# Performance work log

Measured on AMD Instinct MI355X. Metric: run time of the kernel, lower is better.

Reference implementation:

```python
import jax, jax.numpy as jnp
import numpy as np

V = 32000   # input_size (vocab)
H = 768     # hidden_size
C = 256     # condition_size
HC = H + C  # h_c_size
L = 2048    # sequence length


def _lstm_step(x, h, c, W_ih, W_hh, b_ih, b_hh):
    # PyTorch LSTM gate order: i, f, g, o
    gates = x @ W_ih.T + b_ih + h @ W_hh.T + b_hh  # [4*HC]
    i, f, g, o = jnp.split(gates, 4)
    c_new = jax.nn.sigmoid(f) * c + jax.nn.sigmoid(i) * jnp.tanh(g)
    h_new = jax.nn.sigmoid(o) * jnp.tanh(c_new)
    return h_new, c_new


def setup_inputs() -> dict:
    key = jax.random.key(0)
    ks = iter(jax.random.split(key, 40))
    p = lambda shape: (jax.random.normal(next(ks), shape, dtype=jnp.float32) * 0.02)
    inp = {
        "input": jax.random.randint(next(ks), (1, L), 0, V, dtype=jnp.int64),
        "condition": jax.random.randint(next(ks), (1,), 0, 4, dtype=jnp.int64),
        "eps_h": jax.random.normal(next(ks), (H,), dtype=jnp.float32),
        "eps_c": jax.random.normal(next(ks), (H,), dtype=jnp.float32),
        "kld_weight": jax.random.uniform(next(ks), (1,), dtype=jnp.float32),
        # encoder params
        "enc_embed": p((V, HC)),
        "enc_cond_embed": p((4, C)),
        "enc_W_ih": p((4 * HC, HC)), "enc_W_hh": p((4 * HC, HC)),
        "enc_b_ih": p((4 * HC,)), "enc_b_hh": p((4 * HC,)),
        "fc_mh_w": p((H, HC)), "fc_mh_b": p((H,)),
        "fc_lh_w": p((H, HC)), "fc_lh_b": p((H,)),
        "fc_mc_w": p((H, HC)), "fc_mc_b": p((H,)),
        "fc_lc_w": p((H, HC)), "fc_lc_b": p((H,)),
        # decoder params
        "dec_embed": p((V, HC)),
        "dec_cond_embed": p((4, C)),
        "dec_W_ih": p((4 * HC, HC)), "dec_W_hh": p((4 * HC, HC)),
        "dec_b_ih": p((4 * HC,)), "dec_b_hh": p((4 * HC,)),
        "fc_h_w": p((H, HC)), "fc_h_b": p((H,)),
        "fc_c_w": p((H, HC)), "fc_c_b": p((H,)),
        "out_w": p((V, HC)), "out_b": p((V,)),
    }
    return inp


def reference(input, condition, eps_h, eps_c, kld_weight,
              enc_embed, enc_cond_embed, enc_W_ih, enc_W_hh, enc_b_ih, enc_b_hh,
              fc_mh_w, fc_mh_b, fc_lh_w, fc_lh_b, fc_mc_w, fc_mc_b, fc_lc_w, fc_lc_b,
              dec_embed, dec_cond_embed, dec_W_ih, dec_W_hh, dec_b_ih, dec_b_hh,
              fc_h_w, fc_h_b, fc_c_w, fc_c_b, out_w, out_b):
    tokens = input[0]          # [L]
    cond = condition[0]

    # ---- Encoder over tokens[1:-1] ----
    x_seq = enc_embed[tokens[1:-1]]              # [L-2, HC]
    c_emb = enc_cond_embed[cond]                 # [C]
    h0 = jnp.concatenate([jnp.zeros((H,), jnp.float32), c_emb])  # [HC]
    c0 = h0

    def enc_step(carry, x):
        h, c = carry
        h, c = _lstm_step(x, h, c, enc_W_ih, enc_W_hh, enc_b_ih, enc_b_hh)
        return (h, c), None

    (hT, cT), _ = jax.lax.scan(enc_step, (h0, c0), x_seq)

    m_h = hT @ fc_mh_w.T + fc_mh_b
    lv_h = hT @ fc_lh_w.T + fc_lh_b
    z_h = eps_h * jnp.exp(lv_h * 0.5) + m_h      # [H]
    m_c = cT @ fc_mc_w.T + fc_mc_b
    lv_c = cT @ fc_lc_w.T + fc_lc_b
    z_c = eps_c * jnp.exp(lv_c * 0.5) + m_c

    kl_h = 0.5 * jnp.sum(m_h ** 2 + jnp.exp(lv_h) - 1.0 - lv_h)
    kl_c = 0.5 * jnp.sum(m_c ** 2 + jnp.exp(lv_c) - 1.0 - lv_c)

    # ---- Decoder, teacher forcing over L-1 steps ----
    dec_x = dec_embed[tokens[:-1]]               # [L-1, HC]
    targets = tokens[1:]                         # [L-1]
    cd = dec_cond_embed[cond]                    # [C]

    def dec_step(carry, xt):
        h, c = carry                             # [H], [H]
        x, tgt = xt
        hc = jnp.concatenate([h, cd])            # [HC]
        cc = jnp.concatenate([c, cd])
        h_new, c_new = _lstm_step(x, hc, cc, dec_W_ih, dec_W_hh, dec_b_ih, dec_b_hh)
        logits = h_new @ out_w.T + out_b         # [V]
        ce = -jax.nn.log_softmax(logits)[tgt]
        h2 = h_new @ fc_h_w.T + fc_h_b
        c2 = c_new @ fc_c_w.T + fc_c_b
        return (h2, c2), ce

    _, ces = jax.lax.scan(dec_step, (z_h, z_c), (dec_x, targets))
    reconst = jnp.mean(ces)
    loss = reconst + (kl_h + kl_c) * kld_weight[0]
    return jnp.stack([loss, reconst, kl_h, kl_c])
```

## Files before the change

kernel.cpp:

```cpp
#include <hip/hip_runtime.h>
#include <math.h>

#define VSZ 32000
#define Hh  768
#define Cc  256
#define HCd 1024
#define G4  4096
#define NSE 2046
#define NSD 2047

#define EB 64
#define ET 512

typedef __attribute__((ext_vector_type(4))) unsigned uint4v;
typedef __attribute__((ext_vector_type(2))) unsigned uint2v;
typedef __attribute__((ext_vector_type(8))) short bf16x8;
typedef __attribute__((ext_vector_type(4))) float f32x4;

__device__ __forceinline__ float sigmoidf_(float x){ return 1.0f/(1.0f+expf(-x)); }

__device__ __forceinline__ float wave_reduce(float v){
#pragma unroll
  for(int o=32;o;o>>=1) v += __shfl_xor(v,o,64);
  return v;
}

__device__ __forceinline__ float redl0(float v){
  int x;
  x=__builtin_amdgcn_update_dpp(0,__float_as_int(v),0xB1,0xf,0xf,true); v+=__int_as_float(x);
  x=__builtin_amdgcn_update_dpp(0,__float_as_int(v),0x4E,0xf,0xf,true); v+=__int_as_float(x);
  v+=__int_as_float(__builtin_amdgcn_ds_swizzle(__float_as_int(v),0x101F));
  v+=__int_as_float(__builtin_amdgcn_ds_swizzle(__float_as_int(v),0x201F));
  v+=__int_as_float(__builtin_amdgcn_ds_swizzle(__float_as_int(v),0x401F));
  v+=__int_as_float(__builtin_amdgcn_readlane(__float_as_int(v),32));
  return v;
}

__device__ __forceinline__ uint4v ld_uc4(const unsigned* p){
  uint4v r;
  asm volatile("global_load_dwordx4 %0, %1, off sc0 sc1\n\ts_waitcnt vmcnt(0)"
               : "=v"(r) : "v"(p) : "memory");
  return r;
}
__device__ __forceinline__ uint2v ld_uc2(const unsigned* p){
  uint2v r;
  asm volatile("global_load_dwordx2 %0, %1, off sc0 sc1\n\ts_waitcnt vmcnt(0)"
               : "=v"(r) : "v"(p) : "memory");
  return r;
}
__device__ __forceinline__ void st_uc4(unsigned* p, uint4v v){
  asm volatile("global_store_dwordx4 %0, %1, off sc0 sc1" :: "v"(p), "v"(v) : "memory");
}
__device__ __forceinline__ void st_uc2(unsigned* p, uint2v v){
  asm volatile("global_store_dwordx2 %0, %1, off sc0 sc1" :: "v"(p), "v"(v) : "memory");
}

__device__ __forceinline__ unsigned pk_bf16(float a, float b){
  unsigned ua=__float_as_uint(a); ua += 0x7fffu + ((ua>>16)&1u);
  unsigned ub=__float_as_uint(b); ub += 0x7fffu + ((ub>>16)&1u);
  return (ua>>16) | (ub & 0xffff0000u);
}

__global__ void k_init3(unsigned* estate, const float* __restrict__ cemb,
                        const int* __restrict__ condp){
  int tid=threadIdx.x;
  int cond=condp[0];
  for(int i=tid;i<HCd;i+=256){
    float v=(i<Hh)?0.f:cemb[cond*Cc+(i-Hh)];
    estate[i]=__float_as_uint(v)&~1u;
    estate[HCd+i]=1u;
  }
}

__global__ __launch_bounds__(256) void k_dconst(const float* __restrict__ Whh,
    const float* __restrict__ fhb, const float* __restrict__ cemb,
    const int* __restrict__ condp, float* __restrict__ cvec){
  int lane=threadIdx.x&63, wv=threadIdx.x>>6;
  int wgid=blockIdx.x*4+wv;
  int cond=condp[0];
  for(int r=wgid;r<G4;r+=256){
    const float* row=Whh+(size_t)r*HCd;
    float s=0.f;
    for(int k=lane;k<Hh;k+=64) s+=row[k]*fhb[k];
    for(int k=lane;k<Cc;k+=64) s+=row[Hh+k]*cemb[cond*Cc+k];
    s=wave_reduce(s);
    if(lane==0) cvec[r]=s;
  }
}

#define GBM 128
#define GBN 128
#define GBK 16

__global__ __launch_bounds__(256) void k_weff(const float* __restrict__ A,
    const float* __restrict__ B, float* __restrict__ Cm){
  __shared__ float As[GBK][GBM];
  __shared__ float Bs[GBK][GBN];
  int tid=threadIdx.x;
  int m0=blockIdx.x*GBM, n0=blockIdx.y*GBN;
  int tm=tid>>4, tn=tid&15;
  float acc[8][8]={};
  for(int k0=0;k0<Hh;k0+=GBK){
#pragma unroll
    for(int u=0;u<2;u++){
      int idx=tid*2+u;
      int row=idx>>2, q=idx&3;
      float4 v=*(const float4*)(A+(size_t)(m0+row)*HCd + k0+q*4);
      As[q*4+0][row]=v.x; As[q*4+1][row]=v.y; As[q*4+2][row]=v.z; As[q*4+3][row]=v.w;
      int kk=idx>>5, nc=idx&31;
      float4 w=*(const float4*)(B+(size_t)(k0+kk)*HCd + n0+nc*4);
      *(float4*)&Bs[kk][nc*4]=w;
    }
    __syncthreads();
#pragma unroll
    for(int kk=0;kk<GBK;kk++){
      float a[8],b[8];
      *(float4*)&a[0]=*(float4*)&As[kk][tm*8]; *(float4*)&a[4]=*(float4*)&As[kk][tm*8+4];
      *(float4*)&b[0]=*(float4*)&Bs[kk][tn*8]; *(float4*)&b[4]=*(float4*)&Bs[kk][tn*8+4];
#pragma unroll
      for(int i=0;i<8;i++)
#pragma unroll
        for(int j=0;j<8;j++) acc[i][j]+=a[i]*b[j];
    }
    __syncthreads();
  }
#pragma unroll
  for(int i=0;i<8;i++)
#pragma unroll
    for(int j=0;j<8;j++)
      Cm[(size_t)(m0+tm*8+i)*HCd + n0+tn*8+j]=acc[i][j];
}

__global__ __launch_bounds__(256) void k_xgemm(
    const float* __restrict__ emb, const float* __restrict__ Wih,
    const float* __restrict__ b1, const float* __restrict__ b2,
    const int* __restrict__ tok, int tshift, int M,
    float* __restrict__ X)
{
  __shared__ float As[GBK][GBM];
  __shared__ float Bs[GBK][GBN];
  int tid=threadIdx.x;
  int m0=blockIdx.x*GBM, n0=blockIdx.y*GBN;
  int tm=tid>>4, tn=tid&15;
  int arow=m0+(tid>>1);
  int atok=(arow<M)?tok[arow+tshift]:0;
  const float* abase=emb+(size_t)atok*HCd+(tid&1)*8;
  const float* bbase=Wih+(size_t)(n0+(tid>>1))*HCd+(tid&1)*8;
  int srow=tid>>1;
  float acc[8][8]={};
  for(int k0=0;k0<HCd;k0+=GBK){
#pragma unroll
    for(int u=0;u<2;u++){
      int q=2*(tid&1)+u;
      float4 v={0,0,0,0};
      if(arow<M) v=*(const float4*)(abase+k0+u*4);
      As[q*4+0][srow]=v.x; As[q*4+1][srow]=v.y; As[q*4+2][srow]=v.z; As[q*4+3][srow]=v.w;
      float4 w=*(const float4*)(bbase+k0+u*4);
      Bs[q*4+0][srow]=w.x; Bs[q*4+1][srow]=w.y; Bs[q*4+2][srow]=w.z; Bs[q*4+3][srow]=w.w;
    }
    __syncthreads();
#pragma unroll
    for(int kk=0;kk<GBK;kk++){
      float a[8],b[8];
      *(float4*)&a[0]=*(float4*)&As[kk][tm*8]; *(float4*)&a[4]=*(float4*)&As[kk][tm*8+4];
      *(float4*)&b[0]=*(float4*)&Bs[kk][tn*8]; *(float4*)&b[4]=*(float4*)&Bs[kk][tn*8+4];
#pragma unroll
      for(int i=0;i<8;i++)
#pragma unroll
        for(int j=0;j<8;j++) acc[i][j]+=a[i]*b[j];
    }
    __syncthreads();
  }
#pragma unroll
  for(int i=0;i<8;i++){
    int m=m0+tm*8+i; if(m>=M) continue;
#pragma unroll
    for(int j=0;j<8;j++){
      int n=n0+tn*8+j;
      X[(size_t)m*G4+n]=acc[i][j]+b1[n]+b2[n];
    }
  }
}

#define TBM 128
#define TBN 128
#define TBK 32

__global__ __launch_bounds__(256) void k_xgemm_mfma(
    const float* __restrict__ emb, const float* __restrict__ Wih,
    const float* __restrict__ b1, const float* __restrict__ b2,
    const int* __restrict__ tok, int M, float* __restrict__ X)
{
  __shared__ ushort As[TBM*TBK];
  __shared__ ushort Bs[TBN*TBK];
  int tid=threadIdx.x;
  int m0=blockIdx.x*TBM, n0=blockIdx.y*TBN;
  int wid=tid>>6, lane=tid&63;
  int wm=wid>>1, wn=wid&1;
  int r15=lane&15, g=lane>>4;
  f32x4 acc[4][4]={};
  int srow=tid>>1, shalf=tid&1;
  int arow=m0+srow;
  int atok=(arow<M)?tok[arow]:0;
  const float* aptr=emb+(size_t)atok*HCd + shalf*16;
  const float* bptr=Wih+(size_t)(n0+srow)*HCd + shalf*16;
  bool aok=arow<M;
  float bj[4];
#pragma unroll
  for(int j=0;j<4;j++){ int n=n0+wn*64+j*16+r15; bj[j]=b1[n]+b2[n]; }

  for(int k0=0;k0<HCd;k0+=TBK){
    float4 va0={0,0,0,0},va1={0,0,0,0},va2={0,0,0,0},va3={0,0,0,0};
    if(aok){
      va0=*(const float4*)(aptr+k0);   va1=*(const float4*)(aptr+k0+4);
      va2=*(const float4*)(aptr+k0+8); va3=*(const float4*)(aptr+k0+12);
    }
    float4 vb0=*(const float4*)(bptr+k0),   vb1=*(const float4*)(bptr+k0+4);
    float4 vb2=*(const float4*)(bptr+k0+8), vb3=*(const float4*)(bptr+k0+12);
    uint4v pa0={pk_bf16(va0.x,va0.y),pk_bf16(va0.z,va0.w),pk_bf16(va1.x,va1.y),pk_bf16(va1.z,va1.w)};
    uint4v pa1={pk_bf16(va2.x,va2.y),pk_bf16(va2.z,va2.w),pk_bf16(va3.x,va3.y),pk_bf16(va3.z,va3.w)};
    uint4v pb0={pk_bf16(vb0.x,vb0.y),pk_bf16(vb0.z,vb0.w),pk_bf16(vb1.x,vb1.y),pk_bf16(vb1.z,vb1.w)};
    uint4v pb1={pk_bf16(vb2.x,vb2.y),pk_bf16(vb2.z,vb2.w),pk_bf16(vb3.x,vb3.y),pk_bf16(vb3.z,vb3.w)};
    int sx=(srow>>1)&3;
    int u0=(shalf*2+0)^sx, u1=(shalf*2+1)^sx;
    *(uint4v*)&As[srow*32+u0*8]=pa0; *(uint4v*)&As[srow*32+u1*8]=pa1;
    *(uint4v*)&Bs[srow*32+u0*8]=pb0; *(uint4v*)&Bs[srow*32+u1*8]=pb1;
    __syncthreads();
    bf16x8 af[4], bf[4];
#pragma unroll
    for(int i=0;i<4;i++){
      int ra=wm*64+i*16+r15;
      af[i]=*(const bf16x8*)&As[ra*32+((g^((ra>>1)&3))<<3)];
      int rb=wn*64+i*16+r15;
      bf[i]=*(const bf16x8*)&Bs[rb*32+((g^((rb>>1)&3))<<3)];
    }
#pragma unroll
    for(int i=0;i<4;i++)
#pragma unroll
      for(int j=0;j<4;j++)
        acc[i][j]=__builtin_amdgcn_mfma_f32_16x16x32_bf16(af[i],bf[j],acc[i][j],0,0,0);
    __syncthreads();
  }
#pragma unroll
  for(int i=0;i<4;i++){
    int grow0=m0+wm*64+i*16+g*4;
#pragma unroll
    for(int j=0;j<4;j++){
      int gcol=n0+wn*64+j*16+r15;
#pragma unroll
      for(int r=0;r<4;r++){
        int grow=grow0+r;
        if(grow<M) X[(size_t)grow*G4+gcol]=acc[i][j][r]+bj[j];
      }
    }
  }
}

__global__ __launch_bounds__(ET,2) void k_enc3(
    const float* __restrict__ Xg,
    const float* __restrict__ Whh,
    unsigned* estate,
    float* hT, float* cT)
{
  __shared__ float hlds[2][HCd];
  const int tid=threadIdx.x, lane=tid&63, wv=tid>>6;
  const int wid=blockIdx.x*8+wv;
  const int j0=wid*2, j1=j0+1;
  float w[8][16];
#pragma unroll
  for(int q=0;q<4;q++)
#pragma unroll
    for(int jj=0;jj<2;jj++){
      const float* p=Whh+(size_t)(q*HCd+j0+jj)*HCd+lane;
#pragma unroll
      for(int e=0;e<16;e++) w[q*2+jj][e]=p[(size_t)e*64];
    }
  float xg[8];
#pragma unroll
  for(int r=0;r<8;r++) xg[r]=Xg[(r>>1)*HCd+j0+(r&1)];
  float c0=0.f,c1=0.f;
  const int i0=tid*2, i1=i0+1;

  for(int s=1;s<=NSE;s++){
    uint2v v;
    unsigned* src=estate+((s-1)&1)*HCd;
    if(s==1){ v.x=src[i0]; v.y=src[i1]; }
    else{
      const unsigned expp=(unsigned)(((s-1)>>1)&1);
      for(;;){
        v=ld_uc2(src+i0);
        if((((v.x^expp)|(v.y^expp))&1u)==0u) break;
        __builtin_amdgcn_s_sleep(1);
      }
    }
    float* hl=hlds[(s-1)&1];
    hl[i0]=__uint_as_float(v.x); hl[i1]=__uint_as_float(v.y);
    __syncthreads();
    if(s==1){ c0=hl[j0]; c1=hl[j1]; }
    float hseg[16];
#pragma unroll
    for(int e=0;e<16;e++) hseg[e]=hl[lane+64*e];
    float d[8];
#pragma unroll
    for(int r=0;r<8;r++){ float sacc=0.f;
#pragma unroll
      for(int e=0;e<16;e++) sacc+=w[r][e]*hseg[e];
      d[r]=sacc; }
#pragma unroll
    for(int r=0;r<8;r++) d[r]=redl0(d[r]);
    float gi0=d[0]+xg[0], gi1=d[1]+xg[1];
    float gf0=d[2]+xg[2], gf1=d[3]+xg[3];
    float gg0=d[4]+xg[4], gg1=d[5]+xg[5];
    float go0=d[6]+xg[6], go1=d[7]+xg[7];
    if(s<NSE){
      const float* px=Xg+(size_t)s*G4;
#pragma unroll
      for(int r=0;r<8;r++) xg[r]=px[(r>>1)*HCd+j0+(r&1)];
    }
    c0=sigmoidf_(gf0)*c0+sigmoidf_(gi0)*tanhf(gg0);
    float h0=sigmoidf_(go0)*tanhf(c0);
    c1=sigmoidf_(gf1)*c1+sigmoidf_(gi1)*tanhf(gg1);
    float h1=sigmoidf_(go1)*tanhf(c1);
    unsigned wpar=(unsigned)((s>>1)&1);
    if(lane==0){
      uint2v pk;
      pk.x=(__float_as_uint(h0)&~1u)|wpar;
      pk.y=(__float_as_uint(h1)&~1u)|wpar;
      st_uc2(estate+(s&1)*HCd+j0,pk);
      if(s==NSE){ hT[j0]=h0; hT[j1]=h1; cT[j0]=c0; cT[j1]=c1; }
    }
  }
}

__global__ __launch_bounds__(256) void k_head(
    const float* __restrict__ hT, const float* __restrict__ cT,
    const float* __restrict__ mhw, const float* __restrict__ mhb,
    const float* __restrict__ lhw, const float* __restrict__ lhb,
    const float* __restrict__ mcw, const float* __restrict__ mcb,
    const float* __restrict__ lcw, const float* __restrict__ lcb,
    const float* __restrict__ eps_h, const float* __restrict__ eps_c,
    const float* __restrict__ cemb, const int* __restrict__ condp,
    unsigned* dstate0, float* klh, float* klc)
{
  int i=blockIdx.x;
  int tid=threadIdx.x, lane=tid&63, wv=tid>>6;
  __shared__ float sm[4];
  const float* Wm=(wv==0)?mhw:(wv==1)?lhw:(wv==2)?mcw:lcw;
  const float* vec=(wv<2)?hT:cT;
  const float* row=Wm+(size_t)i*HCd;
  float s=0.f;
  for(int k=lane;k<HCd;k+=64) s+=row[k]*vec[k];
  s=wave_reduce(s);
  if(lane==0) sm[wv]=s;
  __syncthreads();
  if(tid==0){
    float mh=sm[0]+mhb[i], lh=sm[1]+lhb[i];
    float mc=sm[2]+mcb[i], lc=sm[3]+lcb[i];
    float zhv=eps_h[i]*expf(lh*0.5f)+mh;
    float zcv=eps_c[i]*expf(lc*0.5f)+mc;
    dstate0[2*i]  =__float_as_uint(zhv)&~1u;
    dstate0[2*i+1]=__float_as_uint(zcv)&~1u;
    klh[i]=0.5f*(mh*mh+expf(lh)-1.f-lh);
    klc[i]=0.5f*(mc*mc+expf(lc)-1.f-lc);
    if(i<Cc){
      unsigned cu=__float_as_uint(cemb[condp[0]*Cc+i])&~1u;
      dstate0[2*(Hh+i)]=cu; dstate0[2*(Hh+i)+1]=cu;
    }
  }
}

__global__ __launch_bounds__(256) void k_dec0(
    const float* __restrict__ Xg, const float* __restrict__ WhhO,
    const unsigned* __restrict__ dstate0, unsigned* dstate1, float* Hmat)
{
  int tid=threadIdx.x, lane=tid&63, wv=tid>>6;
  int j=blockIdx.x*4+wv;
  float hseg[16];
#pragma unroll
  for(int e=0;e<16;e++) hseg[e]=__uint_as_float(dstate0[2*(lane+64*e)]);
  float g[4];
#pragma unroll
  for(int q=0;q<4;q++){
    const float* p=WhhO+(size_t)(q*HCd+j)*HCd+lane;
    float s=0.f;
#pragma unroll
    for(int e=0;e<16;e++) s+=p[(size_t)e*64]*hseg[e];
    s=wave_reduce(s);
    g[q]=s+Xg[q*HCd+j];
  }
  float cc=__uint_as_float(dstate0[2*j+1]);
  float cn=sigmoidf_(g[1])*cc+sigmoidf_(g[0])*tanhf(g[2]);
  float hn=sigmoidf_(g[3])*tanhf(cn);
  if(lane==0){
    dstate1[2*j]  =__float_as_uint(hn)&~1u;
    dstate1[2*j+1]=__float_as_uint(cn)&~1u;
    Hmat[j]=hn;
  }
}

__global__ __launch_bounds__(ET,2) void k_dec3(
    const float* __restrict__ Xg,
    const float* __restrict__ Weff,
    const float* __restrict__ cvec,
    const float* __restrict__ fccw, const float* __restrict__ fccb,
    const float* __restrict__ cemb, const int* __restrict__ condp,
    unsigned* dstate, float* __restrict__ Hmat)
{
  __shared__ float hlds[2][HCd];
  __shared__ float clds[2][HCd];
  const int tid=threadIdx.x, lane=tid&63, wv=tid>>6;
  const int wid=blockIdx.x*8+wv;
  const int j0=wid*2, j1=j0+1;
  float w[8][16];
#pragma unroll
  for(int q=0;q<4;q++)
#pragma unroll
    for(int jj=0;jj<2;jj++){
      const float* p=Weff+(size_t)(q*HCd+j0+jj)*HCd+lane;
#pragma unroll
      for(int e=0;e<16;e++) w[q*2+jj][e]=p[(size_t)e*64];
    }
  const bool hasf=(j0<Hh);
  float fcc0[16], fcc1[16];
  if(hasf){
    const float* p0=fccw+(size_t)j0*HCd+lane;
    const float* p1=fccw+(size_t)j1*HCd+lane;
#pragma unroll
    for(int e=0;e<16;e++){ fcc0[e]=p0[(size_t)e*64]; fcc1[e]=p1[(size_t)e*64]; }
  } else {
#pragma unroll
    for(int e=0;e<16;e++){ fcc0[e]=0.f; fcc1[e]=0.f; }
  }
  float fb0=hasf?fccb[j0]:0.f, fb1=hasf?fccb[j1]:0.f;
  int cond=condp[0];
  float cd0=hasf?0.f:cemb[cond*Cc+(j0-Hh)];
  float cd1=hasf?0.f:cemb[cond*Cc+(j1-Hh)];
  float cv[8];
#pragma unroll
  for(int r=0;r<8;r++) cv[r]=cvec[(r>>1)*HCd+j0+(r&1)];
  float xg[8];
  { const float* px=Xg+(size_t)1*G4;
#pragma unroll
    for(int r=0;r<8;r++) xg[r]=px[(r>>1)*HCd+j0+(r&1)]; }
  const int i0=tid*2, i1=i0+1;

  for(int s=2;s<=NSD;s++){
    uint4v v;
    unsigned* st=dstate+((s-1)&1)*2*HCd;
    if(s==2){ v=*(const uint4v*)(st+4*tid); }
    else{
      const unsigned expp=(unsigned)(((s-1)>>1)&1);
      for(;;){
        v=ld_uc4(st+4*tid);
        if((((v.x^expp)|(v.y^expp)|(v.z^expp)|(v.w^expp))&1u)==0u) break;
        __builtin_amdgcn_s_sleep(1);
      }
    }
    float* hl=hlds[(s-1)&1]; float* cl=clds[(s-1)&1];
    hl[i0]=__uint_as_float(v.x); cl[i0]=__uint_as_float(v.y);
    hl[i1]=__uint_as_float(v.z); cl[i1]=__uint_as_float(v.w);
    __syncthreads();
    float hseg[16], cseg[16];
#pragma unroll
    for(int e=0;e<16;e++){ hseg[e]=hl[lane+64*e]; cseg[e]=cl[lane+64*e]; }
    float d[8]; float s8=0.f, s9=0.f;
#pragma unroll
    for(int r=0;r<8;r++){ float sacc=0.f;
#pragma unroll
      for(int e=0;e<16;e++) sacc+=w[r][e]*hseg[e];
      d[r]=sacc; }
#pragma unroll
    for(int r=0;r<8;r++) d[r]=redl0(d[r]);
    if(hasf){
#pragma unroll
      for(int e=0;e<16;e++){ s8+=fcc0[e]*cseg[e]; s9+=fcc1[e]*cseg[e]; }
      s8=redl0(s8); s9=redl0(s9);
    }
    float gi0=d[0]+xg[0]+cv[0], gi1=d[1]+xg[1]+cv[1];
    float gf0=d[2]+xg[2]+cv[2], gf1=d[3]+xg[3]+cv[3];
    float gg0=d[4]+xg[4]+cv[4], gg1=d[5]+xg[5]+cv[5];
    float go0=d[6]+xg[6]+cv[6], go1=d[7]+xg[7]+cv[7];
    if(s<NSD){
      const float* px=Xg+(size_t)s*G4;
#pragma unroll
      for(int r=0;r<8;r++) xg[r]=px[(r>>1)*HCd+j0+(r&1)];
    }
    float cc0=hasf?(s8+fb0):cd0;
    float cc1=hasf?(s9+fb1):cd1;
    float cn0=sigmoidf_(gf0)*cc0+sigmoidf_(gi0)*tanhf(gg0);
    float hn0=sigmoidf_(go0)*tanhf(cn0);
    float cn1=sigmoidf_(gf1)*cc1+sigmoidf_(gi1)*tanhf(gg1);
    float hn1=sigmoidf_(go1)*tanhf(cn1);
    unsigned wpar=(unsigned)((s>>1)&1);
    if(lane==0){
      uint4v pk;
      pk.x=(__float_as_uint(hn0)&~1u)|wpar;
      pk.y=(__float_as_uint(cn0)&~1u)|wpar;
      pk.z=(__float_as_uint(hn1)&~1u)|wpar;
      pk.w=(__float_as_uint(cn1)&~1u)|wpar;
      st_uc4(dstate+(s&1)*2*HCd+2*j0,pk);
      Hmat[(size_t)(s-1)*HCd+j0]=hn0; Hmat[(size_t)(s-1)*HCd+j1]=hn1;
    }
  }
}

__global__ __launch_bounds__(256) void k_cvtB(const float* __restrict__ B,
    unsigned* __restrict__ Bb){
  size_t idx=(size_t)blockIdx.x*256+threadIdx.x;
  size_t total=(size_t)VSZ*HCd/4;
  for(size_t i=idx;i<total;i+=(size_t)gridDim.x*256){
    float4 v=*(const float4*)(B+i*4);
    Bb[i*2]  =pk_bf16(v.x,v.y);
    Bb[i*2+1]=pk_bf16(v.z,v.w);
  }
}

__global__ __launch_bounds__(256) void k_gemm2(
    const float* __restrict__ A, const ushort* __restrict__ Bb,
    const float* __restrict__ bias, float* __restrict__ Cm, int M)
{
  __shared__ ushort As[TBM*TBK];
  __shared__ ushort Bs[TBN*TBK];
  int tid=threadIdx.x;
  int m0=blockIdx.x*TBM, n0=blockIdx.y*TBN;
  int wid=tid>>6, lane=tid&63;
  int wm=wid>>1, wn=wid&1;
  int r15=lane&15, g=lane>>4;
  f32x4 acc[4][4]={};
  int srow=tid>>1, shalf=tid&1;
  const float*  aptr=A +(size_t)(m0+srow)*HCd + shalf*16;
  const ushort* bptr=Bb+(size_t)(n0+srow)*HCd + shalf*16;
  bool aok=(m0+srow)<M;
  float bj[4];
#pragma unroll
  for(int j=0;j<4;j++) bj[j]=bias[n0+wn*64+j*16+r15];

  for(int k0=0;k0<HCd;k0+=TBK){
    float4 va0={0,0,0,0},va1={0,0,0,0},va2={0,0,0,0},va3={0,0,0,0};
    if(aok){
      va0=*(const float4*)(aptr+k0);   va1=*(const float4*)(aptr+k0+4);
      va2=*(const float4*)(aptr+k0+8); va3=*(const float4*)(aptr+k0+12);
    }
    uint4v qb0=*(const uint4v*)(bptr+k0);
    uint4v qb1=*(const uint4v*)(bptr+k0+8);
    uint4v pa0={pk_bf16(va0.x,va0.y),pk_bf16(va0.z,va0.w),pk_bf16(va1.x,va1.y),pk_bf16(va1.z,va1.w)};
    uint4v pa1={pk_bf16(va2.x,va2.y),pk_bf16(va2.z,va2.w),pk_bf16(va3.x,va3.y),pk_bf16(va3.z,va3.w)};
    int sx=(srow>>1)&3;
    int u0=(shalf*2+0)^sx, u1=(shalf*2+1)^sx;
    *(uint4v*)&As[srow*32+u0*8]=pa0; *(uint4v*)&As[srow*32+u1*8]=pa1;
    *(uint4v*)&Bs[srow*32+u0*8]=qb0; *(uint4v*)&Bs[srow*32+u1*8]=qb1;
    __syncthreads();
    bf16x8 af[4], bf[4];
#pragma unroll
    for(int i=0;i<4;i++){
      int ra=wm*64+i*16+r15;
      af[i]=*(const bf16x8*)&As[ra*32+((g^((ra>>1)&3))<<3)];
      int rb=wn*64+i*16+r15;
      bf[i]=*(const bf16x8*)&Bs[rb*32+((g^((rb>>1)&3))<<3)];
    }
#pragma unroll
    for(int i=0;i<4;i++)
#pragma unroll
      for(int j=0;j<4;j++)
        acc[i][j]=__builtin_amdgcn_mfma_f32_16x16x32_bf16(af[i],bf[j],acc[i][j],0,0,0);
    __syncthreads();
  }
#pragma unroll
  for(int i=0;i<4;i++){
    int grow0=m0+wm*64+i*16+g*4;
#pragma unroll
    for(int j=0;j<4;j++){
      int gcol=n0+wn*64+j*16+r15;
#pragma unroll
      for(int r=0;r<4;r++){
        int grow=grow0+r;
        if(grow<M) Cm[(size_t)grow*VSZ+gcol]=acc[i][j][r]+bj[j];
      }
    }
  }
}

__global__ __launch_bounds__(256) void k_gemm_mfma(
    const float* __restrict__ A, const float* __restrict__ B,
    const float* __restrict__ bias, float* __restrict__ Cm, int M)
{
  __shared__ ushort As[TBM*TBK];
  __shared__ ushort Bs[TBN*TBK];
  int tid=threadIdx.x;
  int m0=blockIdx.x*TBM, n0=blockIdx.y*TBN;
  int wid=tid>>6, lane=tid&63;
  int wm=wid>>1, wn=wid&1;
  int r15=lane&15, g=lane>>4;
  f32x4 acc[4][4]={};
  int srow=tid>>1, shalf=tid&1;
  const float* aptr=A+(size_t)(m0+srow)*HCd + shalf*16;
  const float* bptr=B+(size_t)(n0+srow)*HCd + shalf*16;
  bool aok=(m0+srow)<M;
  float bj[4];
#pragma unroll
  for(int j=0;j<4;j++) bj[j]=bias[n0+wn*64+j*16+r15];

  for(int k0=0;k0<HCd;k0+=TBK){
    float4 va0={0,0,0,0},va1={0,0,0,0},va2={0,0,0,0},va3={0,0,0,0};
    if(aok){
      va0=*(const float4*)(aptr+k0);   va1=*(const float4*)(aptr+k0+4);
      va2=*(const float4*)(aptr+k0+8); va3=*(const float4*)(aptr+k0+12);
    }
    float4 vb0=*(const float4*)(bptr+k0),   vb1=*(const float4*)(bptr+k0+4);
    float4 vb2=*(const float4*)(bptr+k0+8), vb3=*(const float4*)(bptr+k0+12);
    uint4v pa0={pk_bf16(va0.x,va0.y),pk_bf16(va0.z,va0.w),pk_bf16(va1.x,va1.y),pk_bf16(va1.z,va1.w)};
    uint4v pa1={pk_bf16(va2.x,va2.y),pk_bf16(va2.z,va2.w),pk_bf16(va3.x,va3.y),pk_bf16(va3.z,va3.w)};
    uint4v pb0={pk_bf16(vb0.x,vb0.y),pk_bf16(vb0.z,vb0.w),pk_bf16(vb1.x,vb1.y),pk_bf16(vb1.z,vb1.w)};
    uint4v pb1={pk_bf16(vb2.x,vb2.y),pk_bf16(vb2.z,vb2.w),pk_bf16(vb3.x,vb3.y),pk_bf16(vb3.z,vb3.w)};
    int sx=(srow>>1)&3;
    int u0=(shalf*2+0)^sx, u1=(shalf*2+1)^sx;
    *(uint4v*)&As[srow*32+u0*8]=pa0; *(uint4v*)&As[srow*32+u1*8]=pa1;
    *(uint4v*)&Bs[srow*32+u0*8]=pb0; *(uint4v*)&Bs[srow*32+u1*8]=pb1;
    __syncthreads();
    bf16x8 af[4], bf[4];
#pragma unroll
    for(int i=0;i<4;i++){
      int ra=wm*64+i*16+r15;
      af[i]=*(const bf16x8*)&As[ra*32+((g^((ra>>1)&3))<<3)];
      int rb=wn*64+i*16+r15;
      bf[i]=*(const bf16x8*)&Bs[rb*32+((g^((rb>>1)&3))<<3)];
    }
#pragma unroll
    for(int i=0;i<4;i++)
#pragma unroll
      for(int j=0;j<4;j++)
        acc[i][j]=__builtin_amdgcn_mfma_f32_16x16x32_bf16(af[i],bf[j],acc[i][j],0,0,0);
    __syncthreads();
  }
#pragma unroll
  for(int i=0;i<4;i++){
    int grow0=m0+wm*64+i*16+g*4;
#pragma unroll
    for(int j=0;j<4;j++){
      int gcol=n0+wn*64+j*16+r15;
#pragma unroll
      for(int r=0;r<4;r++){
        int grow=grow0+r;
        if(grow<M) Cm[(size_t)grow*VSZ+gcol]=acc[i][j][r]+bj[j];
      }
    }
  }
}

__global__ __launch_bounds__(256) void k_ce(const float* __restrict__ logits,
    const int* __restrict__ tok, int base, float* __restrict__ ce)
{
  int r=blockIdx.x;
  const float* row=logits+(size_t)r*VSZ;
  int tid=threadIdx.x, lane=tid&63, wv=tid>>6;
  float m=-1e30f, s=0.f;
  for(int i=tid;i<VSZ;i+=256){
    float v=row[i];
    if(v>m){ s=s*__expf(m-v)+1.f; m=v; }
    else s+=__expf(v-m);
  }
#pragma unroll
  for(int o=32;o;o>>=1){
    float mo=__shfl_xor(m,o,64), so=__shfl_xor(s,o,64);
    float mn=fmaxf(m,mo);
    s=s*__expf(m-mn)+so*__expf(mo-mn);
    m=mn;
  }
  __shared__ float smm[4], sms[4];
  if(lane==0){ smm[wv]=m; sms[wv]=s; }
  __syncthreads();
  if(tid==0){
    float M2=fmaxf(fmaxf(smm[0],smm[1]),fmaxf(smm[2],smm[3]));
    float S2=sms[0]*__expf(smm[0]-M2)+sms[1]*__expf(smm[1]-M2)
            +sms[2]*__expf(smm[2]-M2)+sms[3]*__expf(smm[3]-M2);
    int tgt=tok[base+r+1];
    ce[base+r]=M2+logf(S2)-row[tgt];
  }
}

__global__ __launch_bounds__(256) void k_final(const float* __restrict__ ce,
    const float* __restrict__ klh, const float* __restrict__ klc,
    const float* __restrict__ kldw, float* __restrict__ outp)
{
  int tid=threadIdx.x, lane=tid&63, wv=tid>>6;
  float s0=0,s1=0,s2=0;
  for(int i=tid;i<NSD;i+=256) s0+=ce[i];
  for(int i=tid;i<Hh;i+=256){ s1+=klh[i]; s2+=klc[i]; }
  s0=wave_reduce(s0); s1=wave_reduce(s1); s2=wave_reduce(s2);
  __shared__ float sm[3][4];
  if(lane==0){ sm[0][wv]=s0; sm[1][wv]=s1; sm[2][wv]=s2; }
  __syncthreads();
  if(tid==0){
    float ces=sm[0][0]+sm[0][1]+sm[0][2]+sm[0][3];
    float kh =sm[1][0]+sm[1][1]+sm[1][2]+sm[1][3];
    float kc =sm[2][0]+sm[2][1]+sm[2][2]+sm[2][3];
    float rec=ces/(float)NSD;
    outp[0]=rec+(kh+kc)*kldw[0];
    outp[1]=rec; outp[2]=kh; outp[3]=kc;
  }
}

extern "C" void kernel_launch(void* const* d_in, const int* in_sizes, int n_in,
                              void* d_out, int out_size, void* d_ws, size_t ws_size,
                              hipStream_t stream) {
  const int*   tok   =(const int*)  d_in[0];
  const int*   cond  =(const int*)  d_in[1];
  const float* eps_h =(const float*)d_in[2];
  const float* eps_c =(const float*)d_in[3];
  const float* kldw  =(const float*)d_in[4];
  const float* enc_embed=(const float*)d_in[5];
  const float* enc_cemb =(const float*)d_in[6];
  const float* enc_Wih  =(const float*)d_in[7];
  const float* enc_Whh  =(const float*)d_in[8];
  const float* enc_bih  =(const float*)d_in[9];
  const float* enc_bhh  =(const float*)d_in[10];
  const float* fc_mh_w=(const float*)d_in[11];
  const float* fc_mh_b=(const float*)d_in[12];
  const float* fc_lh_w=(const float*)d_in[13];
  const float* fc_lh_b=(const float*)d_in[14];
  const float* fc_mc_w=(const float*)d_in[15];
  const float* fc_mc_b=(const float*)d_in[16];
  const float* fc_lc_w=(const float*)d_in[17];
  const float* fc_lc_b=(const float*)d_in[18];
  const float* dec_embed=(const float*)d_in[19];
  const float* dec_cemb =(const float*)d_in[20];
  const float* dec_Wih  =(const float*)d_in[21];
  const float* dec_Whh  =(const float*)d_in[22];
  const float* dec_bih  =(const float*)d_in[23];
  const float* dec_bhh  =(const float*)d_in[24];
  const float* fc_h_w=(const float*)d_in[25];
  const float* fc_h_b=(const float*)d_in[26];
  const float* fc_c_w=(const float*)d_in[27];
  const float* fc_c_b=(const float*)d_in[28];
  const float* out_w=(const float*)d_in[29];
  const float* out_b=(const float*)d_in[30];

  float* ws=(float*)d_ws;
  size_t off=0;
  unsigned* estate=(unsigned*)(ws+off); off+=2*HCd;
  unsigned* dstate=(unsigned*)(ws+off); off+=4*HCd;
  float* cvec=ws+off; off+=G4;
  float* Weff=ws+off; off+=(size_t)G4*HCd;
  float* hT  =ws+off; off+=HCd;
  float* cT  =ws+off; off+=HCd;
  float* klh =ws+off; off+=Hh;
  float* klc =ws+off; off+=Hh;
  float* Hmat=ws+off; off+=(size_t)NSD*HCd;
  float* ce  =ws+off; off+=2048;
  size_t avail=ws_size/4;
  size_t xa_sz=(size_t)NSE*G4, xb_sz=(size_t)NSD*G4;
  size_t wb_sz=(size_t)VSZ*HCd/2;
  float* XA=ws+off;
  bool dual=(off+xa_sz+xb_sz)<=avail;
  float* XB=dual?(XA+xa_sz):XA;
  bool wbok=dual && (off+xa_sz+xb_sz+wb_sz)<=avail;
  unsigned* wB=(unsigned*)(XB+xb_sz);
  size_t region=(avail>off)?(avail-off):0;
  int chunk=256;
  if(!dual){
    if((size_t)chunk*VSZ>region){ chunk=(int)(region/(size_t)VSZ); if(chunk<1)chunk=1; }
  }
  float* lbuf=XA;

  k_init3<<<1,256,0,stream>>>(estate,enc_cemb,cond);
  k_dconst<<<64,256,0,stream>>>(dec_Whh,fc_h_b,dec_cemb,cond,cvec);
  { dim3 g(G4/GBM, HCd/GBN);
    k_weff<<<g,256,0,stream>>>(dec_Whh,fc_h_w,Weff); }
  { dim3 g((NSE+GBM-1)/GBM, G4/GBN);
    k_xgemm<<<g,256,0,stream>>>(enc_embed,enc_Wih,enc_bih,enc_bhh,tok,1,NSE,XA); }
  if(dual){
    dim3 g((NSD+TBM-1)/TBM, G4/TBN);
    k_xgemm_mfma<<<g,256,0,stream>>>(dec_embed,dec_Wih,dec_bih,dec_bhh,tok,NSD,XB);
  }
  if(wbok) k_cvtB<<<2048,256,0,stream>>>(out_w,wB);
  k_enc3<<<EB,ET,0,stream>>>(XA,enc_Whh,estate,hT,cT);
  k_head<<<Hh,256,0,stream>>>(hT,cT,fc_mh_w,fc_mh_b,fc_lh_w,fc_lh_b,
                              fc_mc_w,fc_mc_b,fc_lc_w,fc_lc_b,
                              eps_h,eps_c,dec_cemb,cond,dstate,klh,klc);
  if(!dual){
    dim3 g((NSD+TBM-1)/TBM, G4/TBN);
    k_xgemm_mfma<<<g,256,0,stream>>>(dec_embed,dec_Wih,dec_bih,dec_bhh,tok,NSD,XB);
  }
  k_dec0<<<256,256,0,stream>>>(XB,dec_Whh,dstate,dstate+2*HCd,Hmat);
  k_dec3<<<EB,ET,0,stream>>>(XB,Weff,cvec,fc_c_w,fc_c_b,dec_cemb,cond,dstate,Hmat);
  for(int base=0;base<NSD;base+=chunk){
    int rows=NSD-base; if(rows>chunk) rows=chunk;
    dim3 g((rows+TBM-1)/TBM, VSZ/TBN);
    if(wbok) k_gemm2<<<g,256,0,stream>>>(Hmat+(size_t)base*HCd,(const ushort*)wB,out_b,lbuf,rows);
    else     k_gemm_mfma<<<g,256,0,stream>>>(Hmat+(size_t)base*HCd,out_w,out_b,lbuf,rows);
    k_ce<<<rows,256,0,stream>>>(lbuf,tok,base,ce);
  }
  k_final<<<1,256,0,stream>>>(ce,klh,klc,kldw,(float*)d_out);
}
```

Measured before the change: 13.61 ms.

## Overlap decoder precompute GEMMs with encoder recurrence in one fused launch

The encoder recurrence kernel is launched with extra blocks beyond the 64 that run the serial LSTM. The extra blocks use idle CUs to run the decoder's independent precompute: the constant vector, the Weff GEMM, the decoder input GEMM and the bf16 conversion of out_w, all sharing one shared-memory union. The head kernel now writes z_h/z_c to plain float buffers, and the logits chunk size grows to reuse the freed XA/XB space. The risk is that the helper blocks contend for memory bandwidth and L2 with the latency-bound recurrence, and that the larger shared-memory footprint lowers occupancy.

```diff
diff --git a/kernel.cpp b/kernel.cpp
--- a/kernel.cpp
+++ b/kernel.cpp
@@ -11,6 +11,7 @@
 
 #define EB 64
 #define ET 512
+#define FGRID 256
 
 typedef __attribute__((ext_vector_type(4))) unsigned uint4v;
 typedef __attribute__((ext_vector_type(2))) unsigned uint2v;
@@ -24,7 +25,6 @@
   for(int o=32;o;o>>=1) v += __shfl_xor(v,o,64);
   return v;
 }
-
 __device__ __forceinline__ float redl0(float v){
   int x;
   x=__builtin_amdgcn_update_dpp(0,__float_as_int(v),0xB1,0xf,0xf,true); v+=__int_as_float(x);
@@ -36,23 +36,23 @@
   return v;
 }
 
+__device__ __forceinline__ uint2v ld_uc2(const unsigned* p){
+  uint2v r;
+  asm volatile("global_load_dwordx2 %0, %1, off sc0 sc1\n\ts_waitcnt vmcnt(0)"
+               : "=v"(r) : "v"(p) : "memory");
+  return r;
+}
 __device__ __forceinline__ uint4v ld_uc4(const unsigned* p){
   uint4v r;
   asm volatile("global_load_dwordx4 %0, %1, off sc0 sc1\n\ts_waitcnt vmcnt(0)"
                : "=v"(r) : "v"(p) : "memory");
   return r;
 }
-__device__ __forceinline__ uint2v ld_uc2(const unsigned* p){
-  uint2v r;
-  asm volatile("global_load_dwordx2 %0, %1, off sc0 sc1\n\ts_waitcnt vmcnt(0)"
-               : "=v"(r) : "v"(p) : "memory");
-  return r;
+__device__ __forceinline__ void st_uc2(unsigned* p, uint2v v){
+  asm volatile("global_store_dwordx2 %0, %1, off sc0 sc1" :: "v"(p), "v"(v) : "memory");
 }
 __device__ __forceinline__ void st_uc4(unsigned* p, uint4v v){
   asm volatile("global_store_dwordx4 %0, %1, off sc0 sc1" :: "v"(p), "v"(v) : "memory");
-}
-__device__ __forceinline__ void st_uc2(unsigned* p, uint2v v){
-  asm volatile("global_store_dwordx2 %0, %1, off sc0 sc1" :: "v"(p), "v"(v) : "memory");
 }
 
 __device__ __forceinline__ unsigned pk_bf16(float a, float b){
@@ -61,8 +61,8 @@
   return (ua>>16) | (ub & 0xffff0000u);
 }
 
-__global__ void k_init3(unsigned* estate, const float* __restrict__ cemb,
-                        const int* __restrict__ condp){
+__global__ void k_init9(unsigned* estate, unsigned* dstate,
+                        const float* __restrict__ cemb, const int* __restrict__ condp){
   int tid=threadIdx.x;
   int cond=condp[0];
   for(int i=tid;i<HCd;i+=256){
@@ -70,15 +70,156 @@
     estate[i]=__float_as_uint(v)&~1u;
     estate[HCd+i]=1u;
   }
-}
-
-__global__ __launch_bounds__(256) void k_dconst(const float* __restrict__ Whh,
+  for(int i=tid;i<2*HCd;i+=256) dstate[i]=0u;
+}
+
+#define GBM 128
+#define GBN 128
+#define GBK 16
+#define TBM 128
+#define TBN 128
+#define TBK 32
+
+struct SmU {
+  union {
+    float hlds[2][HCd];
+    struct { float As[GBK][GBM]; float Bs[GBK][GBN]; } wf;
+    struct { ushort As[TBM*TBK]; ushort Bs[TBN*TBK]; } xd;
+  } u;
+};
+
+__device__ void weff_unit(int u, const float* __restrict__ A,
+    const float* __restrict__ B, float* __restrict__ Cm, SmU& sm, int tid){
+  int m0=(u>>3)*GBM, n0=(u&7)*GBN;
+  int tm=tid>>4, tn=tid&15;
+  float acc[8][8]={};
+  for(int k0=0;k0<Hh;k0+=GBK){
+    if(tid<256){
+#pragma unroll
+      for(int uu=0;uu<2;uu++){
+        int idx=tid*2+uu;
+        int row=idx>>2, q=idx&3;
+        float4 v=*(const float4*)(A+(size_t)(m0+row)*HCd + k0+q*4);
+        sm.u.wf.As[q*4+0][row]=v.x; sm.u.wf.As[q*4+1][row]=v.y;
+        sm.u.wf.As[q*4+2][row]=v.z; sm.u.wf.As[q*4+3][row]=v.w;
+        int kk=idx>>5, nc=idx&31;
+        float4 w=*(const float4*)(B+(size_t)(k0+kk)*HCd + n0+nc*4);
+        *(float4*)&sm.u.wf.Bs[kk][nc*4]=w;
+      }
+    }
+    __syncthreads();
+    if(tid<256){
+#pragma unroll
+      for(int kk=0;kk<GBK;kk++){
+        float a[8],b[8];
+        *(float4*)&a[0]=*(float4*)&sm.u.wf.As[kk][tm*8]; *(float4*)&a[4]=*(float4*)&sm.u.wf.As[kk][tm*8+4];
+        *(float4*)&b[0]=*(float4*)&sm.u.wf.Bs[kk][tn*8]; *(float4*)&b[4]=*(float4*)&sm.u.wf.Bs[kk][tn*8+4];
+#pragma unroll
+        for(int i=0;i<8;i++)
+#pragma unroll
+          for(int j=0;j<8;j++) acc[i][j]+=a[i]*b[j];
+      }
+    }
+    __syncthreads();
+  }
+  if(tid<256){
+#pragma unroll
+    for(int i=0;i<8;i++)
+#pragma unroll
+      for(int j=0;j<8;j++)
+        Cm[(size_t)(m0+tm*8+i)*HCd + n0+tn*8+j]=acc[i][j];
+  }
+}
+
+__device__ void xdec_unit(int q, const float* __restrict__ emb,
+    const float* __restrict__ Wih, const float* __restrict__ b1,
+    const float* __restrict__ b2, const int* __restrict__ tok,
+    float* __restrict__ X, SmU& sm, int tid){
+  int m0=(q>>5)*TBM, n0=(q&31)*TBN;
+  int wid=tid>>6, lane=tid&63;
+  int wm=wid>>1, wn=wid&1;
+  int r15=lane&15, g=lane>>4;
+  f32x4 acc[4][4]={};
+  int srow=tid>>1, shalf=tid&1;
+  int arow=m0+srow;
+  bool act=(tid<256);
+  int atok=(act&&arow<NSD)?tok[arow]:0;
+  const float* aptr=emb+(size_t)atok*HCd + shalf*16;
+  const float* bptr=Wih+(size_t)(n0+srow)*HCd + shalf*16;
+  bool aok=act&&(arow<NSD);
+  float bj[4];
+  if(act){
+#pragma unroll
+    for(int j=0;j<4;j++){ int n=n0+wn*64+j*16+r15; bj[j]=b1[n]+b2[n]; }
+  }
+  for(int k0=0;k0<HCd;k0+=TBK){
+    if(act){
+      float4 va0={0,0,0,0},va1={0,0,0,0},va2={0,0,0,0},va3={0,0,0,0};
+      if(aok){
+        va0=*(const float4*)(aptr+k0);   va1=*(const float4*)(aptr+k0+4);
+        va2=*(const float4*)(aptr+k0+8); va3=*(const float4*)(aptr+k0+12);
+      }
+      float4 vb0=*(const float4*)(bptr+k0),   vb1=*(const float4*)(bptr+k0+4);
+      float4 vb2=*(const float4*)(bptr+k0+8), vb3=*(const float4*)(bptr+k0+12);
+      uint4v pa0={pk_bf16(va0.x,va0.y),pk_bf16(va0.z,va0.w),pk_bf16(va1.x,va1.y),pk_bf16(va1.z,va1.w)};
+      uint4v pa1={pk_bf16(va2.x,va2.y),pk_bf16(va2.z,va2.w),pk_bf16(va3.x,va3.y),pk_bf16(va3.z,va3.w)};
+      uint4v pb0={pk_bf16(vb0.x,vb0.y),pk_bf16(vb0.z,vb0.w),pk_bf16(vb1.x,vb1.y),pk_bf16(vb1.z,vb1.w)};
+      uint4v pb1={pk_bf16(vb2.x,vb2.y),pk_bf16(vb2.z,vb2.w),pk_bf16(vb3.x,vb3.y),pk_bf16(vb3.z,vb3.w)};
+      int sx=(srow>>1)&3;
+      int u0=(shalf*2+0)^sx, u1=(shalf*2+1)^sx;
+      *(uint4v*)&sm.u.xd.As[srow*32+u0*8]=pa0; *(uint4v*)&sm.u.xd.As[srow*32+u1*8]=pa1;
+      *(uint4v*)&sm.u.xd.Bs[srow*32+u0*8]=pb0; *(uint4v*)&sm.u.xd.Bs[srow*32+u1*8]=pb1;
+    }
+    __syncthreads();
+    if(act){
+      bf16x8 af[4], bf[4];
+#pragma unroll
+      for(int i=0;i<4;i++){
+        int ra=wm*64+i*16+r15;
+        af[i]=*(const bf16x8*)&sm.u.xd.As[ra*32+((g^((ra>>1)&3))<<3)];
+        int rb=wn*64+i*16+r15;
+        bf[i]=*(const bf16x8*)&sm.u.xd.Bs[rb*32+((g^((rb>>1)&3))<<3)];
+      }
+#pragma unroll
+      for(int i=0;i<4;i++)
+#pragma unroll
+        for(int j=0;j<4;j++)
+          acc[i][j]=__builtin_amdgcn_mfma_f32_16x16x32_bf16(af[i],bf[j],acc[i][j],0,0,0);
+    }
+    __syncthreads();
+  }
+  if(act){
+#pragma unroll
+    for(int i=0;i<4;i++){
+      int grow0=m0+wm*64+i*16+g*4;
+#pragma unroll
+      for(int j=0;j<4;j++){
+        int gcol=n0+wn*64+j*16+r15;
+#pragma unroll
+        for(int r=0;r<4;r++){
+          int grow=grow0+r;
+          if(grow<NSD) X[(size_t)grow*G4+gcol]=acc[i][j][r]+bj[j];
+        }
+      }
+    }
+  }
+}
+
+__device__ void cvtb_unit(int i, const float* __restrict__ B,
+    unsigned* __restrict__ Bb, int tid){
+  size_t base=(size_t)i*128000u;
+  for(size_t x=base+tid; x<base+128000u; x+=ET){
+    float4 v=*(const float4*)(B+x*4);
+    Bb[x*2]  =pk_bf16(v.x,v.y);
+    Bb[x*2+1]=pk_bf16(v.z,v.w);
+  }
+}
+
+__device__ void dconst_unit(int i, const float* __restrict__ Whh,
     const float* __restrict__ fhb, const float* __restrict__ cemb,
-    const int* __restrict__ condp, float* __restrict__ cvec){
-  int lane=threadIdx.x&63, wv=threadIdx.x>>6;
-  int wgid=blockIdx.x*4+wv;
-  int cond=condp[0];
-  for(int r=wgid;r<G4;r+=256){
+    int cond, float* __restrict__ cvec, int tid){
+  int lane=tid&63, wv=tid>>6;
+  for(int r=i*256+wv; r<i*256+256; r+=8){
     const float* row=Whh+(size_t)r*HCd;
     float s=0.f;
     for(int k=lane;k<Hh;k+=64) s+=row[k]*fhb[k];
@@ -86,49 +227,6 @@
     s=wave_reduce(s);
     if(lane==0) cvec[r]=s;
   }
-}
-
-#define GBM 128
-#define GBN 128
-#define GBK 16
-
-__global__ __launch_bounds__(256) void k_weff(const float* __restrict__ A,
-    const float* __restrict__ B, float* __restrict__ Cm){
-  __shared__ float As[GBK][GBM];
-  __shared__ float Bs[GBK][GBN];
-  int tid=threadIdx.x;
-  int m0=blockIdx.x*GBM, n0=blockIdx.y*GBN;
-  int tm=tid>>4, tn=tid&15;
-  float acc[8][8]={};
-  for(int k0=0;k0<Hh;k0+=GBK){
-#pragma unroll
-    for(int u=0;u<2;u++){
-      int idx=tid*2+u;
-      int row=idx>>2, q=idx&3;
-      float4 v=*(const float4*)(A+(size_t)(m0+row)*HCd + k0+q*4);
-      As[q*4+0][row]=v.x; As[q*4+1][row]=v.y; As[q*4+2][row]=v.z; As[q*4+3][row]=v.w;
-      int kk=idx>>5, nc=idx&31;
-      float4 w=*(const float4*)(B+(size_t)(k0+kk)*HCd + n0+nc*4);
-      *(float4*)&Bs[kk][nc*4]=w;
-    }
-    __syncthreads();
-#pragma unroll
-    for(int kk=0;kk<GBK;kk++){
-      float a[8],b[8];
-      *(float4*)&a[0]=*(float4*)&As[kk][tm*8]; *(float4*)&a[4]=*(float4*)&As[kk][tm*8+4];
-      *(float4*)&b[0]=*(float4*)&Bs[kk][tn*8]; *(float4*)&b[4]=*(float4*)&Bs[kk][tn*8+4];
-#pragma unroll
-      for(int i=0;i<8;i++)
-#pragma unroll
-        for(int j=0;j<8;j++) acc[i][j]+=a[i]*b[j];
-    }
-    __syncthreads();
-  }
-#pragma unroll
-  for(int i=0;i<8;i++)
-#pragma unroll
-    for(int j=0;j<8;j++)
-      Cm[(size_t)(m0+tm*8+i)*HCd + n0+tn*8+j]=acc[i][j];
 }
 
 __global__ __launch_bounds__(256) void k_xgemm(
@@ -181,10 +279,6 @@
     }
   }
 }
-
-#define TBM 128
-#define TBN 128
-#define TBK 32
 
 __global__ __launch_bounds__(256) void k_xgemm_mfma(
     const float* __restrict__ emb, const float* __restrict__ Wih,
@@ -208,7 +302,6 @@
   float bj[4];
 #pragma unroll
   for(int j=0;j<4;j++){ int n=n0+wn*64+j*16+r15; bj[j]=b1[n]+b2[n]; }
-
   for(int k0=0;k0<HCd;k0+=TBK){
     float4 va0={0,0,0,0},va1={0,0,0,0},va2={0,0,0,0},va3={0,0,0,0};
     if(aok){
@@ -256,15 +349,38 @@
   }
 }
 
-__global__ __launch_bounds__(ET,2) void k_enc3(
-    const float* __restrict__ Xg,
-    const float* __restrict__ Whh,
-    unsigned* estate,
-    float* hT, float* cT)
-{
-  __shared__ float hlds[2][HCd];
+__global__ __launch_bounds__(ET,2) void k_encF(
+    const float* __restrict__ Xg, const float* __restrict__ Whh,
+    unsigned* estate, float* hT, float* cT,
+    const float* __restrict__ dWhh, const float* __restrict__ fhw,
+    float* __restrict__ Weff,
+    const float* __restrict__ demb, const float* __restrict__ dWih,
+    const float* __restrict__ dbih, const float* __restrict__ dbhh,
+    const int* __restrict__ tok, float* __restrict__ XB,
+    const float* __restrict__ outw, unsigned* __restrict__ wB,
+    const float* __restrict__ fhb, const float* __restrict__ dcemb,
+    const int* __restrict__ condp, float* __restrict__ cvec,
+    int do_xdec, int do_cvtb)
+{
+  __shared__ SmU sm;
   const int tid=threadIdx.x, lane=tid&63, wv=tid>>6;
-  const int wid=blockIdx.x*8+wv;
+  const int bid=blockIdx.x;
+
+  if(bid>=EB){
+    int cond=condp[0];
+    int n_x=do_xdec?512:0, n_c=do_cvtb?64:0;
+    int total=16+256+n_x+n_c;
+    for(int u=bid-EB; u<total; u+=FGRID-EB){
+      if(u<16) dconst_unit(u,dWhh,fhb,dcemb,cond,cvec,tid);
+      else if(u<272) weff_unit(u-16,dWhh,fhw,Weff,sm,tid);
+      else if(u<272+n_x) xdec_unit(u-272,demb,dWih,dbih,dbhh,tok,XB,sm,tid);
+      else cvtb_unit(u-272-n_x,outw,wB,tid);
+      __syncthreads();
+    }
+    return;
+  }
+
+  const int wid=bid*8+wv;
   const int j0=wid*2, j1=j0+1;
   float w[8][16];
 #pragma unroll
@@ -293,7 +409,7 @@
         __builtin_amdgcn_s_sleep(1);
       }
     }
-    float* hl=hlds[(s-1)&1];
+    float* hl=sm.u.hlds[(s-1)&1];
     hl[i0]=__uint_as_float(v.x); hl[i1]=__uint_as_float(v.y);
     __syncthreads();
     if(s==1){ c0=hl[j0]; c1=hl[j1]; }
@@ -340,7 +456,7 @@
     const float* __restrict__ lcw, const float* __restrict__ lcb,
     const float* __restrict__ eps_h, const float* __restrict__ eps_c,
     const float* __restrict__ cemb, const int* __restrict__ condp,
-    unsigned* dstate0, float* klh, float* klc)
+    float* zh, float* zc, float* klh, float* klc)
 {
   int i=blockIdx.x;
   int tid=threadIdx.x, lane=tid&63, wv=tid>>6;
@@ -356,28 +472,27 @@
   if(tid==0){
     float mh=sm[0]+mhb[i], lh=sm[1]+lhb[i];
     float mc=sm[2]+mcb[i], lc=sm[3]+lcb[i];
-    float zhv=eps_h[i]*expf(lh*0.5f)+mh;
-    float zcv=eps_c[i]*expf(lc*0.5f)+mc;
-    dstate0[2*i]  =__float_as_uint(zhv)&~1u;
-    dstate0[2*i+1]=__float_as_uint(zcv)&~1u;
+    zh[i]=eps_h[i]*expf(lh*0.5f)+mh;
+    zc[i]=eps_c[i]*expf(lc*0.5f)+mc;
     klh[i]=0.5f*(mh*mh+expf(lh)-1.f-lh);
     klc[i]=0.5f*(mc*mc+expf(lc)-1.f-lc);
     if(i<Cc){
-      unsigned cu=__float_as_uint(cemb[condp[0]*Cc+i])&~1u;
-      dstate0[2*(Hh+i)]=cu; dstate0[2*(Hh+i)+1]=cu;
+      float cd=cemb[condp[0]*Cc+i];
+      zh[Hh+i]=cd; zc[Hh+i]=cd;
     }
   }
 }
 
 __global__ __launch_bounds__(256) void k_dec0(
     const float* __restrict__ Xg, const float* __restrict__ WhhO,
-    const unsigned* __restrict__ dstate0, unsigned* dstate1, float* Hmat)
+    const float* __restrict__ zh, const float* __restrict__ zc,
+    unsigned* dstate1, float* Hmat)
 {
   int tid=threadIdx.x, lane=tid&63, wv=tid>>6;
   int j=blockIdx.x*4+wv;
   float hseg[16];
 #pragma unroll
-  for(int e=0;e<16;e++) hseg[e]=__uint_as_float(dstate0[2*(lane+64*e)]);
+  for(int e=0;e<16;e++) hseg[e]=zh[lane+64*e];
   float g[4];
 #pragma unroll
   for(int q=0;q<4;q++){
@@ -388,7 +503,7 @@
     s=wave_reduce(s);
     g[q]=s+Xg[q*HCd+j];
   }
-  float cc=__uint_as_float(dstate0[2*j+1]);
+  float cc=zc[j];
   float cn=sigmoidf_(g[1])*cc+sigmoidf_(g[0])*tanhf(g[2]);
   float hn=sigmoidf_(g[3])*tanhf(cn);
   if(lane==0){
@@ -398,9 +513,8 @@
   }
 }
 
-__global__ __launch_bounds__(ET,2) void k_dec3(
-    const float* __restrict__ Xg,
-    const float* __restrict__ Weff,
+__global__ __launch_bounds__(ET,2) void k_dec9(
+    const float* __restrict__ Xg, const float* __restrict__ Weff,
     const float* __restrict__ cvec,
     const float* __restrict__ fccw, const float* __restrict__ fccb,
     const float* __restrict__ cemb, const int* __restrict__ condp,
@@ -504,17 +618,6 @@
   }
 }
 
-__global__ __launch_bounds__(256) void k_cvtB(const float* __restrict__ B,
-    unsigned* __restrict__ Bb){
-  size_t idx=(size_t)blockIdx.x*256+threadIdx.x;
-  size_t total=(size_t)VSZ*HCd/4;
-  for(size_t i=idx;i<total;i+=(size_t)gridDim.x*256){
-    float4 v=*(const float4*)(B+i*4);
-    Bb[i*2]  =pk_bf16(v.x,v.y);
-    Bb[i*2+1]=pk_bf16(v.z,v.w);
-  }
-}
-
 __global__ __launch_bounds__(256) void k_gemm2(
     const float* __restrict__ A, const ushort* __restrict__ Bb,
     const float* __restrict__ bias, float* __restrict__ Cm, int M)
@@ -599,7 +702,6 @@
   float bj[4];
 #pragma unroll
   for(int j=0;j<4;j++) bj[j]=bias[n0+wn*64+j*16+r15];
-
   for(int k0=0;k0<HCd;k0+=TBK){
     float4 va0={0,0,0,0},va1={0,0,0,0},va2={0,0,0,0},va3={0,0,0,0};
     if(aok){
@@ -743,6 +845,8 @@
   float* Weff=ws+off; off+=(size_t)G4*HCd;
   float* hT  =ws+off; off+=HCd;
   float* cT  =ws+off; off+=HCd;
+  float* zh  =ws+off; off+=HCd;
+  float* zc  =ws+off; off+=HCd;
   float* klh =ws+off; off+=Hh;
   float* klc =ws+off; off+=Hh;
   float* Hmat=ws+off; off+=(size_t)NSD*HCd;
@@ -756,33 +860,32 @@
   bool wbok=dual && (off+xa_sz+xb_sz+wb_sz)<=avail;
   unsigned* wB=(unsigned*)(XB+xb_sz);
   size_t region=(avail>off)?(avail-off):0;
-  int chunk=256;
-  if(!dual){
+  int chunk;
+  if(dual){
+    chunk=(int)((xa_sz+xb_sz)/(size_t)VSZ); if(chunk>512)chunk=512;
+  } else {
+    chunk=256;
     if((size_t)chunk*VSZ>region){ chunk=(int)(region/(size_t)VSZ); if(chunk<1)chunk=1; }
   }
   float* lbuf=XA;
 
-  k_init3<<<1,256,0,stream>>>(estate,enc_cemb,cond);
-  k_dconst<<<64,256,0,stream>>>(dec_Whh,fc_h_b,dec_cemb,cond,cvec);
-  { dim3 g(G4/GBM, HCd/GBN);
-    k_weff<<<g,256,0,stream>>>(dec_Whh,fc_h_w,Weff); }
+  k_init9<<<1,256,0,stream>>>(estate,dstate,enc_cemb,cond);
   { dim3 g((NSE+GBM-1)/GBM, G4/GBN);
     k_xgemm<<<g,256,0,stream>>>(enc_embed,enc_Wih,enc_bih,enc_bhh,tok,1,NSE,XA); }
-  if(dual){
-    dim3 g((NSD+TBM-1)/TBM, G4/TBN);
-    k_xgemm_mfma<<<g,256,0,stream>>>(dec_embed,dec_Wih,dec_bih,dec_bhh,tok,NSD,XB);
-  }
-  if(wbok) k_cvtB<<<2048,256,0,stream>>>(out_w,wB);
-  k_enc3<<<EB,ET,0,stream>>>(XA,enc_Whh,estate,hT,cT);
+  k_encF<<<FGRID,ET,0,stream>>>(XA,enc_Whh,estate,hT,cT,
+                                dec_Whh,fc_h_w,Weff,
+                                dec_embed,dec_Wih,dec_bih,dec_bhh,tok,XB,
+                                out_w,wB,fc_h_b,dec_cemb,cond,cvec,
+                                dual?1:0, wbok?1:0);
   k_head<<<Hh,256,0,stream>>>(hT,cT,fc_mh_w,fc_mh_b,fc_lh_w,fc_lh_b,
                               fc_mc_w,fc_mc_b,fc_lc_w,fc_lc_b,
-                              eps_h,eps_c,dec_cemb,cond,dstate,klh,klc);
+                              eps_h,eps_c,dec_cemb,cond,zh,zc,klh,klc);
   if(!dual){
     dim3 g((NSD+TBM-1)/TBM, G4/TBN);
     k_xgemm_mfma<<<g,256,0,stream>>>(dec_embed,dec_Wih,dec_bih,dec_bhh,tok,NSD,XB);
   }
-  k_dec0<<<256,256,0,stream>>>(XB,dec_Whh,dstate,dstate+2*HCd,Hmat);
-  k_dec3<<<EB,ET,0,stream>>>(XB,Weff,cvec,fc_c_w,fc_c_b,dec_cemb,cond,dstate,Hmat);
+  k_dec0<<<256,256,0,stream>>>(XB,dec_Whh,zh,zc,dstate+2*HCd,Hmat);
+  k_dec9<<<EB,ET,0,stream>>>(XB,Weff,cvec,fc_c_w,fc_c_b,dec_cemb,cond,dstate,Hmat);
   for(int base=0;base<NSD;base+=chunk){
     int rows=NSD-base; if(rows>chunk) rows=chunk;
     dim3 g((rows+TBM-1)/TBM, VSZ/TBN);
```

Measured after the change: 13.53 ms. About the same (-0.6%).
